# Kernel optimization log

Hardware: AMD Instinct MI355X
Metric: run time of the kernel (lower is better)

Reference implementation:

```python
import jax, jax.numpy as jnp
import numpy as np

POINTS_PER_UNIT = 64
N_GRID = 4096          # grid points (64 units * 64 ppu)
BATCH = 4
M_TARGET = 4096
C = 16


def setup_inputs() -> dict:
    key = jax.random.key(0)
    k1, k2 = jax.random.split(key)
    span = N_GRID / POINTS_PER_UNIT  # 64 units
    xz = (jnp.arange(N_GRID, dtype=jnp.float32) / POINTS_PER_UNIT)[:, None]  # [N,1]
    x = jax.random.uniform(k1, (BATCH, M_TARGET, 1), dtype=jnp.float32) * span  # [B,M,1]
    z = jax.random.normal(k2, (BATCH, C, N_GRID), dtype=jnp.float32)  # [B,C,N]
    log_scale = jnp.log(jnp.float32(2.0 / POINTS_PER_UNIT))  # scalar param
    return {"xz": xz, "x": x, "z": z, "log_scale": log_scale}


def reference(xz, x, z, log_scale):
    # pairwise squared distances between x [B,M,1] and grid xz [N,1] -> [B,M,N]
    diff = x - xz[None, :, :].transpose(0, 2, 1)  # [B,M,1]-[1,1,N] -> [B,M,N]
    dists2 = diff * diff
    # RBF kernel weights: exp(-0.5 * d2 / scale^2), scale = exp(log_scale)
    weights = jnp.exp(-0.5 * dists2 * jnp.exp(-2.0 * log_scale))  # [B,M,N]
    zt = jnp.swapaxes(z, -1, -2)  # [B,N,C]
    out = jnp.einsum('bmn,bnc->bmc', weights, zt)  # [B,M,C]
    return (xz, out)
```

## Files before the change

kernel.cpp:

```cpp
#include <hip/hip_runtime.h>


#define N_GRID   4096
#define BATCH    4
#define M_TARGET 4096
#define C_CH     16

__global__ __launch_bounds__(256) void setconv_decoder_kernel(
    const float* __restrict__ xz,
    const float* __restrict__ x,
    const float* __restrict__ z,
    const float* __restrict__ log_scale,
    float* __restrict__ out)
{
    const int t = blockIdx.x * 256 + threadIdx.x;

    if (t < N_GRID) out[t] = xz[t];

    const int c  = t & (C_CH - 1);
    const int bm = t >> 4;
    const int b  = bm >> 12;

    const float xv   = x[bm];
    const float ls   = log_scale[0];
    const float coef = -0.5f * __expf(-2.0f * ls);

    int ic = (int)(xv * 64.0f + 0.5f);
    int lo = ic - 32;
    lo = lo < 0 ? 0 : lo;
    lo = lo > (N_GRID - 64) ? (N_GRID - 64) : lo;
    lo &= ~3;

    const float4* __restrict__ zp =
        (const float4*)(z + ((size_t)(b * C_CH + c)) * N_GRID);
    const int q0 = lo >> 2;

    const float inv64 = 0.015625f;
    float acc = 0.0f;
    #pragma unroll
    for (int i = 0; i < 16; ++i) {
        const int n4 = lo + 4 * i;
        const float4 zv = zp[q0 + i];
        const float g = (float)n4 * inv64;
        float d0 = xv - g;
        float d1 = xv - (g + inv64);
        float d2 = xv - (g + 2.0f * inv64);
        float d3 = xv - (g + 3.0f * inv64);
        acc += __expf(coef * d0 * d0) * zv.x;
        acc += __expf(coef * d1 * d1) * zv.y;
        acc += __expf(coef * d2 * d2) * zv.z;
        acc += __expf(coef * d3 * d3) * zv.w;
    }

    out[N_GRID + bm * C_CH + c] = acc;
}

extern "C" void kernel_launch(void* const* d_in, const int* in_sizes, int n_in,
                              void* d_out, int out_size, void* d_ws, size_t ws_size,
                              hipStream_t stream) {
    const float* xz = (const float*)d_in[0];
    const float* x  = (const float*)d_in[1];
    const float* z  = (const float*)d_in[2];
    const float* ls = (const float*)d_in[3];
    float* out = (float*)d_out;

    const int total = BATCH * M_TARGET * C_CH;
    setconv_decoder_kernel<<<dim3(total / 256), dim3(256), 0, stream>>>(
        xz, x, z, ls, out);
}
```

Measured before the change: 69.55 us.

## Map one wavefront per target point with lane-per-grid-point weights and shuffle reductions

Work is remapped so each 64-lane wavefront handles one target point. Each lane computes a single RBF weight for one grid point in the 64-point window, then loops over the 16 channels with coalesced loads and butterfly shuffle reductions. This removes the 16x redundant exponential evaluation, since previously every channel thread recomputed all 64 weights. The cost is many cross-lane shuffles per wave and four times as many threads. The window start is also no longer aligned to 4, so reads become scalar rather than float4.

```diff
diff --git a/kernel.cpp b/kernel.cpp
--- a/kernel.cpp
+++ b/kernel.cpp
@@ -13,46 +13,39 @@
     const float* __restrict__ log_scale,
     float* __restrict__ out)
 {
-    const int t = blockIdx.x * 256 + threadIdx.x;
+    const int tid  = threadIdx.x;
+    const int lane = tid & 63;
+    const int wave = tid >> 6;
+    const int bm   = blockIdx.x * 4 + wave;
+    const int b    = bm >> 12;
 
-    if (t < N_GRID) out[t] = xz[t];
-
-    const int c  = t & (C_CH - 1);
-    const int bm = t >> 4;
-    const int b  = bm >> 12;
+    const int gt = blockIdx.x * 256 + tid;
+    if (gt < N_GRID) out[gt] = xz[gt];
 
     const float xv   = x[bm];
     const float ls   = log_scale[0];
     const float coef = -0.5f * __expf(-2.0f * ls);
 
-    int ic = (int)(xv * 64.0f + 0.5f);
-    int lo = ic - 32;
-    lo = lo < 0 ? 0 : lo;
-    lo = lo > (N_GRID - 64) ? (N_GRID - 64) : lo;
-    lo &= ~3;
+    int lo = (int)(xv * 64.0f + 0.5f) - 32;
+    lo = lo < 0 ? 0 : (lo > (N_GRID - 64) ? (N_GRID - 64) : lo);
 
-    const float4* __restrict__ zp =
-        (const float4*)(z + ((size_t)(b * C_CH + c)) * N_GRID);
-    const int q0 = lo >> 2;
+    const float d = xv - (float)(lo + lane) * 0.015625f;
+    const float w = __expf(coef * d * d);
 
-    const float inv64 = 0.015625f;
-    float acc = 0.0f;
+    const float* __restrict__ zb = z + ((size_t)b * C_CH) * N_GRID + lo;
+
+    float res = 0.0f;
     #pragma unroll
-    for (int i = 0; i < 16; ++i) {
-        const int n4 = lo + 4 * i;
-        const float4 zv = zp[q0 + i];
-        const float g = (float)n4 * inv64;
-        float d0 = xv - g;
-        float d1 = xv - (g + inv64);
-        float d2 = xv - (g + 2.0f * inv64);
-        float d3 = xv - (g + 3.0f * inv64);
-        acc += __expf(coef * d0 * d0) * zv.x;
-        acc += __expf(coef * d1 * d1) * zv.y;
-        acc += __expf(coef * d2 * d2) * zv.z;
-        acc += __expf(coef * d3 * d3) * zv.w;
+    for (int c = 0; c < C_CH; ++c) {
+        float p = w * zb[(size_t)c * N_GRID + lane];
+        #pragma unroll
+        for (int off = 32; off > 0; off >>= 1)
+            p += __shfl_xor(p, off, 64);
+        if (lane == c) res = p;
     }
 
-    out[N_GRID + bm * C_CH + c] = acc;
+    if (lane < C_CH)
+        out[N_GRID + bm * C_CH + lane] = res;
 }
 
 extern "C" void kernel_launch(void* const* d_in, const int* in_sizes, int n_in,
@@ -64,7 +57,7 @@
     const float* ls = (const float*)d_in[3];
     float* out = (float*)d_out;
 
-    const int total = BATCH * M_TARGET * C_CH;
-    setconv_decoder_kernel<<<dim3(total / 256), dim3(256), 0, stream>>>(
+    const int n_bm = BATCH * M_TARGET;
+    setconv_decoder_kernel<<<dim3(n_bm / 4), dim3(256), 0, stream>>>(
         xz, x, z, ls, out);
 }
```

Result: slower. 76.42 us (+9.9%).
